# Performance work log

Hardware: AMD Instinct MI355X
Metric: run time of the kernel (lower is better)

Reference implementation:

```python
import jax, jax.numpy as jnp
import numpy as np

NUM_HEADS = 8
HEAD_DIM = 96
SCALE = HEAD_DIM ** -0.5
STRIDE_Q = (1, 2, 2)
STRIDE_KV = (1, 8, 8)
PAD = [(1, 1), (1, 1), (1, 1)]  # kernel 3 -> padding = 3//2 = 1


def _gelu_pool(t, w, stride, thw):
    """_pre_attention_pool -> GELU -> depthwise Conv3d -> _post_attention_pool.

    t: [B, H, L, hd] flattened tokens; thw = (T, Hs, Ws) with L = T*Hs*Ws.
    Returns pooled [B, H, L', hd] and new thw.
    """
    B, NH, L, C = t.shape
    T, Hs, Ws = thw
    x = t.reshape(B * NH, T, Hs, Ws, C).transpose(0, 4, 1, 2, 3)  # [B*NH, C, T, Hs, Ws]
    x = jax.nn.gelu(x, approximate=False)  # torch F.gelu default (erf)
    x = jax.lax.conv_general_dilated(
        x, w, window_strides=stride, padding=PAD,
        dimension_numbers=('NCDHW', 'OIDHW', 'NCDHW'),
        feature_group_count=C)  # depthwise: groups = head_dim
    new_thw = (x.shape[2], x.shape[3], x.shape[4])
    Lp = new_thw[0] * new_thw[1] * new_thw[2]
    x = x.reshape(B, NH, C, Lp).transpose(0, 1, 3, 2)  # [B, NH, L', C]
    return x, new_thw


def setup_inputs() -> dict:
    key = jax.random.key(0)
    ks = jax.random.split(key, 8)
    B, T, Hs, Ws, C = 2, 8, 56, 56, 768
    L = T * Hs * Ws
    s = 0.02
    return {
        'x': jax.random.normal(ks[0], (B, L, C), jnp.float32),
        'qkv_w': jax.random.normal(ks[1], (3 * C, C), jnp.float32) * s,
        'qkv_b': jnp.zeros((3 * C,), jnp.float32),
        'proj_w': jax.random.normal(ks[2], (C, C), jnp.float32) * s,
        'proj_b': jnp.zeros((C,), jnp.float32),
        'pool_q_w': jax.random.normal(ks[3], (HEAD_DIM, 1, 3, 3, 3), jnp.float32) * 0.1,
        'pool_k_w': jax.random.normal(ks[4], (HEAD_DIM, 1, 3, 3, 3), jnp.float32) * 0.1,
        'pool_v_w': jax.random.normal(ks[5], (HEAD_DIM, 1, 3, 3, 3), jnp.float32) * 0.1,
        't_size': T, 'h_size': Hs, 'w_size': Ws,
    }


def reference(x, qkv_w, qkv_b, proj_w, proj_b, pool_q_w, pool_k_w, pool_v_w,
              t_size, h_size, w_size):
    B, N, C = x.shape
    # fused qkv projection -> [3, B, heads, N, head_dim]
    qkv = (x @ qkv_w.T + qkv_b).reshape(B, N, 3, NUM_HEADS, C // NUM_HEADS)
    qkv = qkv.transpose(2, 0, 3, 1, 4)
    q, k, v = qkv[0], qkv[1], qkv[2]

    thw = (t_size, h_size, w_size)
    q, q_thw = _gelu_pool(q, pool_q_w, STRIDE_Q, thw)
    k, _ = _gelu_pool(k, pool_k_w, STRIDE_KV, thw)
    v, _ = _gelu_pool(v, pool_v_w, STRIDE_KV, thw)

    attn = jax.nn.softmax((q * SCALE) @ jnp.swapaxes(k, -2, -1), axis=-1)
    Nq = q.shape[2]
    out = (attn @ v + q)  # residual_pool=True (iMViT)
    out = out.transpose(0, 2, 1, 3).reshape(B, Nq, C)
    out = out @ proj_w.T + proj_b
    return out
```

## Files before the change

kernel.cpp:

```cpp
#include <hip/hip_runtime.h>
#include <cstdint>

#define NH 8
#define HD 96
#define CDIM 768
#define BQ 2
#define T0 8
#define H0 56
#define W0 56
#define L0 (T0*H0*W0)
#define HP_Q 28
#define WP_Q 28
#define LQ (T0*HP_Q*WP_Q)
#define HP_K 7
#define WP_K 7
#define LK (T0*HP_K*WP_K)
#define LKP 416
#define SCALE 0.10206207261596577f
#define NYC 20
#define MKV 6400

typedef __bf16 bf16;
typedef bf16 bf16x4 __attribute__((ext_vector_type(4)));
typedef bf16 bf16x8 __attribute__((ext_vector_type(8)));
typedef float f32x4 __attribute__((ext_vector_type(4)));
typedef float f4 __attribute__((ext_vector_type(4)));

#define GPTR(x) ((const __attribute__((address_space(1))) void*)(x))
#define LPTR(x) ((__attribute__((address_space(3))) void*)(x))

__device__ __forceinline__ float fast_gelu(float x) {
    float z = __builtin_fabsf(x) * 0.7071067811865476f;
    float p = 1.f + z*(0.278393f + z*(0.230389f + z*(0.000972f + z*0.078108f)));
    p = p * p;
    p = p * p;
    float e = 1.f - __builtin_amdgcn_rcpf(p);
    float erfv = (x < 0.f) ? -e : e;
    return 0.5f * x * (1.f + erfv);
}

#define NW4 442368
#define NP4 147456
__global__ void cvt_w(const f4* __restrict__ wq, const f4* __restrict__ wp,
                      bf16x4* __restrict__ wqo, bf16x4* __restrict__ wpo) {
    const long total = NW4 + NP4;
    long stride = (long)gridDim.x * blockDim.x;
    for (long i = (long)blockIdx.x * blockDim.x + threadIdx.x; i < total; i += stride) {
        f4 v; bf16x4* o;
        if (i < NW4) { v = wq[i]; o = wqo + i; }
        else         { v = wp[i - NW4]; o = wpo + (i - NW4); }
        bf16x4 t;
        t[0] = (bf16)v[0]; t[1] = (bf16)v[1]; t[2] = (bf16)v[2]; t[3] = (bf16)v[3];
        *o = t;
    }
}

__device__ __forceinline__ int cmap(int i) {
    return ((i + 1) / 3) * 8 + (i + 1) % 3 - 1;
}

template<int MODE>
__global__ __launch_bounds__(256) void gemm_f32a(
    const float* __restrict__ A, const bf16* __restrict__ B,
    const float* __restrict__ bias, bf16* __restrict__ Out,
    int M, int N, int K, int NBN)
{
    __shared__ uint8_t sh[2*24576];
    const int tid = threadIdx.x;
    const int lane = tid & 63;
    const int w = tid >> 6;
    const int wr = w >> 1, wc = w & 1;
    const int g = lane >> 4;
    const int ar = lane & 15;

    const int nwg = gridDim.x;
    const int q_ = nwg >> 3, r_ = nwg & 7;
    const int xcd = blockIdx.x & 7, off = blockIdx.x >> 3;
    const int swz = (xcd < r_ ? xcd*(q_+1) : r_*(q_+1) + (xcd - r_)*q_) + off;
    const long bn = swz % NBN, bm = swz / NBN;

    f32x4 acc[4][4];
#pragma unroll
    for (int i = 0; i < 4; ++i)
#pragma unroll
        for (int j = 0; j < 4; ++j) acc[i][j] = (f32x4){0.f,0.f,0.f,0.f};

    const int arow_s = tid >> 3;
    const int csa = (tid & 7) ^ (arow_s & 7);
    long aoff[4];
#pragma unroll
    for (int s = 0; s < 4; ++s) {
        int rA = (int)bm*128 + s*32 + arow_s;
        if (MODE == 2) {
            int b = rA / 3200; int r = rA - b*3200;
            int t = r / 400;  int rr = r - t*400;
            int yi = rr / NYC, xi = rr - yi*NYC;
            aoff[s] = ((long)b*L0 + (t*H0 + cmap(yi))*W0 + cmap(xi)) * (long)K;
        } else {
            aoff[s] = (long)rA * K;
        }
    }
    const int brow_s = tid >> 2;
    const int csb = (tid & 3) ^ ((tid >> 3) & 3);
    const bf16* Bg = B + (bn*128 + brow_s)*(long)K + csb*8;

    auto stage = [&](int buf, int kt) {
        uint8_t* base = sh + buf*24576;
#pragma unroll
        for (int s = 0; s < 4; ++s)
            __builtin_amdgcn_global_load_lds(GPTR(A + aoff[s] + kt*32 + csa*4),
                LPTR(base + s*4096 + tid*16), 16, 0, 0);
#pragma unroll
        for (int s = 0; s < 2; ++s)
            __builtin_amdgcn_global_load_lds(GPTR(Bg + (long)kt*32 + (long)s*64*K),
                LPTR(base + 16384 + s*4096 + tid*16), 16, 0, 0);
    };
    auto compute = [&](int buf) {
        const float* ldsA = (const float*)(sh + buf*24576);
        const bf16* ldsB = (const bf16*)(sh + buf*24576 + 16384);
        bf16x8 af[4], bfr[4];
#pragma unroll
        for (int i = 0; i < 4; ++i) {
            int R = wr*64 + i*16 + ar;
            f32x4 lo = *(const f32x4*)&ldsA[R*32 + (((2*g    ) ^ (R & 7))*4)];
            f32x4 hi = *(const f32x4*)&ldsA[R*32 + (((2*g + 1) ^ (R & 7))*4)];
            bf16x8 t;
            t[0] = (bf16)lo[0]; t[1] = (bf16)lo[1]; t[2] = (bf16)lo[2]; t[3] = (bf16)lo[3];
            t[4] = (bf16)hi[0]; t[5] = (bf16)hi[1]; t[6] = (bf16)hi[2]; t[7] = (bf16)hi[3];
            af[i] = t;
        }
#pragma unroll
        for (int j = 0; j < 4; ++j) {
            int R = wc*64 + j*16 + ar;
            bfr[j] = *(const bf16x8*)&ldsB[R*32 + ((g ^ ((R >> 1) & 3))*8)];
        }
        __builtin_amdgcn_s_setprio(1);
#pragma unroll
        for (int i = 0; i < 4; ++i)
#pragma unroll
            for (int j = 0; j < 4; ++j)
                acc[i][j] = __builtin_amdgcn_mfma_f32_16x16x32_bf16(af[i], bfr[j], acc[i][j], 0, 0, 0);
        __builtin_amdgcn_s_setprio(0);
    };

    const int nkt = K / 32;
    stage(0, 0);
    for (int kt = 0; kt < nkt; ++kt) {
        if (kt + 1 < nkt) {
            stage((kt + 1) & 1, kt + 1);
            asm volatile("s_waitcnt vmcnt(6)" ::: "memory");
        } else {
            asm volatile("s_waitcnt vmcnt(0)" ::: "memory");
        }
        __builtin_amdgcn_s_barrier();
        __builtin_amdgcn_sched_barrier(0);
        compute(kt & 1);
        __builtin_amdgcn_sched_barrier(0);
        __builtin_amdgcn_s_barrier();
    }

    bf16* tls = (bf16*)sh;
#pragma unroll
    for (int j = 0; j < 4; ++j) {
        const int colb = (int)bn*128 + wc*64 + j*16;
        const int lcol = wc*64 + j*16 + ar;
        const float bcol = bias[colb + ar];
#pragma unroll
        for (int i = 0; i < 4; ++i) {
            int lrow0 = wr*64 + i*16 + (g << 2);
#pragma unroll
            for (int r = 0; r < 4; ++r)
                tls[(lrow0 + r)*136 + lcol] = (bf16)fast_gelu(acc[i][j][r] + bcol);
        }
    }
    __syncthreads();
#pragma unroll
    for (int it = 0; it < 8; ++it) {
        int idx = it*256 + tid;
        int mloc = idx >> 4;
        int ck = idx & 15;
        bf16x8 v = *(const bf16x8*)&tls[mloc*136 + ck*8];
        int m = (int)bm*128 + mloc;
        int col = (int)bn*128 + ck*8;
        if (MODE == 0) {
            int nh = col / HD;
            int c = col - nh*HD;
            int bflag = m >= L0;
            int l = m - (bflag ? L0 : 0);
            size_t addr = ((size_t)(bflag*8 + nh)*L0 + l)*HD + c;
            *(bf16x8*)&Out[addr] = v;
        } else {
            int part = col / 768;
            int cb = col - part*768;
            int nh = cb / HD;
            int c = cb - nh*HD;
            int b = m / 3200; int r = m - b*3200;
            size_t addr = ((size_t)(part*16 + b*8 + nh)*3200 + r)*HD + c;
            *(bf16x8*)&Out[addr] = v;
        }
    }
}

__global__ __launch_bounds__(256) void gemm_proj(
    const bf16* __restrict__ A, const bf16* __restrict__ B,
    const float* __restrict__ bias, float* __restrict__ Out,
    int M, int N, int K, int NBN)
{
    __shared__ bf16 sh[2*16384];
    const int tid = threadIdx.x;
    const int lane = tid & 63;
    const int w = tid >> 6;
    const int wr = w >> 1, wc = w & 1;

    const int nwg = gridDim.x;
    const int q_ = nwg >> 3, r_ = nwg & 7;
    const int xcd = blockIdx.x & 7, off = blockIdx.x >> 3;
    const int swz = (xcd < r_ ? xcd*(q_+1) : r_*(q_+1) + (xcd - r_)*q_) + off;
    const long bn = swz % NBN, bm = swz / NBN;

    f32x4 acc[4][4];
#pragma unroll
    for (int i = 0; i < 4; ++i)
#pragma unroll
        for (int j = 0; j < 4; ++j) acc[i][j] = (f32x4){0.f,0.f,0.f,0.f};

    const int trow = tid >> 3;
    const int tchunk = (tid & 7) ^ (trow & 7);
    const bf16* Ag = A + (bm*128 + trow)*(long)K + tchunk*8;
    const bf16* Bg = B + (bn*128 + trow)*(long)K + tchunk*8;

    const int arow = lane & 15;
    const int g8 = (lane >> 4) * 8;
    const int aswz = (arow & 7) * 8;

    auto stage = [&](int buf, int kt) {
        bf16* ldsA = sh + buf*16384;
        bf16* ldsB = sh + buf*16384 + 8192;
#pragma unroll
        for (int s = 0; s < 4; ++s) {
            __builtin_amdgcn_global_load_lds(GPTR(Ag + (long)kt*64 + (long)s*32*K),
                                             LPTR(ldsA + s*2048 + tid*8), 16, 0, 0);
            __builtin_amdgcn_global_load_lds(GPTR(Bg + (long)kt*64 + (long)s*32*K),
                                             LPTR(ldsB + s*2048 + tid*8), 16, 0, 0);
        }
    };
    auto compute = [&](int buf) {
        const bf16* ldsA = sh + buf*16384;
        const bf16* ldsB = sh + buf*16384 + 8192;
#pragma unroll
        for (int kk = 0; kk < 2; ++kk) {
            bf16x8 af[4], bfr[4];
#pragma unroll
            for (int i = 0; i < 4; ++i)
                af[i] = *(const bf16x8*)&ldsA[(wr*64 + i*16 + arow)*64 + ((kk*32 + g8) ^ aswz)];
#pragma unroll
            for (int j = 0; j < 4; ++j)
                bfr[j] = *(const bf16x8*)&ldsB[(wc*64 + j*16 + arow)*64 + ((kk*32 + g8) ^ aswz)];
            __builtin_amdgcn_s_setprio(1);
#pragma unroll
            for (int i = 0; i < 4; ++i)
#pragma unroll
                for (int j = 0; j < 4; ++j)
                    acc[i][j] = __builtin_amdgcn_mfma_f32_16x16x32_bf16(af[i], bfr[j], acc[i][j], 0, 0, 0);
            __builtin_amdgcn_s_setprio(0);
        }
    };

    const int nkt = K / 64;
    stage(0, 0);
    for (int kt = 0; kt < nkt; ++kt) {
        if (kt + 1 < nkt) {
            stage((kt + 1) & 1, kt + 1);
            asm volatile("s_waitcnt vmcnt(8)" ::: "memory");
        } else {
            asm volatile("s_waitcnt vmcnt(0)" ::: "memory");
        }
        __builtin_amdgcn_s_barrier();
        __builtin_amdgcn_sched_barrier(0);
        compute(kt & 1);
        __builtin_amdgcn_sched_barrier(0);
        __builtin_amdgcn_s_barrier();
    }

#pragma unroll
    for (int j = 0; j < 4; ++j) {
        const int col = (int)bn*128 + wc*64 + j*16 + (lane & 15);
        const float bcol = bias[col];
#pragma unroll
        for (int i = 0; i < 4; ++i) {
            int row0 = (int)bm*128 + wr*64 + i*16 + ((lane>>4)<<2);
#pragma unroll
            for (int r = 0; r < 4; ++r)
                Out[(size_t)(row0 + r)*N + col] = acc[i][j][r] + bcol;
        }
    }
}

__global__ __launch_bounds__(256) void dwconv_q(
    const bf16* __restrict__ in, const float* __restrict__ w,
    bf16* __restrict__ out, int total)
{
    __shared__ float lw[27*HD];
    for (int i = threadIdx.x; i < 27*HD; i += 256) {
        int c = i / 27, tap = i % 27;
        lw[tap*HD + c] = w[i];
    }
    __syncthreads();
    int idx = blockIdx.x*256 + threadIdx.x;
    if (idx >= total) return;
    int c8 = idx % 12;
    int p = idx / 12;
    int xo = p % WP_Q;
    int yo = (p / WP_Q) % HP_Q;
    int bh = p / (WP_Q*HP_Q);
    const bf16* ip = in + (size_t)bh * L0 * HD + c8*8;

    float acc[T0][8];
#pragma unroll
    for (int t = 0; t < T0; ++t)
#pragma unroll
        for (int j = 0; j < 8; ++j) acc[t][j] = 0.f;

#pragma unroll
    for (int dy = 0; dy < 3; ++dy) {
        int y = yo*2 + dy - 1;
        if ((unsigned)y >= (unsigned)H0) continue;
#pragma unroll
        for (int dx = 0; dx < 3; ++dx) {
            int x = xo*2 + dx - 1;
            if ((unsigned)x >= (unsigned)W0) continue;
            float wreg[3][8];
#pragma unroll
            for (int dt = 0; dt < 3; ++dt)
#pragma unroll
                for (int j = 0; j < 8; ++j)
                    wreg[dt][j] = lw[(dt*9 + dy*3 + dx)*HD + c8*8 + j];
            const bf16* colp = ip + ((size_t)(y*W0 + x))*HD;
#pragma unroll
            for (int t = 0; t < T0; ++t) {
                bf16x8 v = *(const bf16x8*)(colp + (size_t)t*H0*W0*HD);
                float f[8];
#pragma unroll
                for (int j = 0; j < 8; ++j) f[j] = (float)v[j];
#pragma unroll
                for (int dt = 0; dt < 3; ++dt) {
                    int to = t - dt + 1;
                    if (to < 0 || to >= T0) continue;
#pragma unroll
                    for (int j = 0; j < 8; ++j)
                        acc[to][j] += wreg[dt][j] * f[j];
                }
            }
        }
    }

#pragma unroll
    for (int to = 0; to < T0; ++to) {
        int l = (to*HP_Q + yo)*WP_Q + xo;
        bf16x8 ov;
#pragma unroll
        for (int j = 0; j < 8; ++j) ov[j] = (bf16)acc[to][j];
        *(bf16x8*)&out[((size_t)bh*LQ + l)*HD + c8*8] = ov;
    }
}

__global__ __launch_bounds__(256) void dwconv_kv_all(
    const bf16* __restrict__ kv, const float* __restrict__ wk,
    const float* __restrict__ wv, bf16* __restrict__ kout, bf16* __restrict__ vtout)
{
    const int seg = blockIdx.x / 40;
    const int lb  = blockIdx.x % 40;
    const float* w = seg ? wv : wk;
    const bf16* in = kv + (size_t)seg * 16 * 3200 * HD;
    __shared__ float lw[27*HD];
    for (int i = threadIdx.x; i < 27*HD; i += 256) {
        int c = i / 27, tap = i % 27;
        lw[tap*HD + c] = w[i];
    }
    __syncthreads();

    if (lb >= 37) {
        int pid = (lb - 37)*256 + threadIdx.x;
        if (seg == 0) {
            for (int e = pid; e < 16*24*96; e += 768) {
                int bh = e / (24*96); int rem = e - bh*24*96;
                int l = LK + rem / 96; int c = rem % 96;
                kout[((size_t)bh*LKP + l)*HD + c] = (bf16)0.f;
            }
        } else {
            for (int e = pid; e < 16*96*24; e += 768) {
                int bh = e / (96*24); int rem = e - bh*96*24;
                int c = rem / 24; int l = LK + rem % 24;
                vtout[((size_t)bh*HD + c)*LKP + l] = (bf16)0.f;
            }
        }
        return;
    }

    int idx = lb*256 + threadIdx.x;
    if (idx >= 16*HP_K*WP_K*12) return;
    int c8 = idx % 12;
    int p = idx / 12;
    int xo = p % WP_K;
    int yo = (p / WP_K) % HP_K;
    int bh = p / (WP_K*HP_K);
    const bf16* ip = in + (size_t)bh * 3200 * HD + c8*8;

    float acc[T0][8];
#pragma unroll
    for (int t = 0; t < T0; ++t)
#pragma unroll
        for (int j = 0; j < 8; ++j) acc[t][j] = 0.f;

#pragma unroll
    for (int dy = 0; dy < 3; ++dy) {
        int yi = 3*yo + dy - 1;
        if ((unsigned)yi >= (unsigned)NYC) continue;
#pragma unroll
        for (int dx = 0; dx < 3; ++dx) {
            int xi = 3*xo + dx - 1;
            if ((unsigned)xi >= (unsigned)NYC) continue;
            float wreg[3][8];
#pragma unroll
            for (int dt = 0; dt < 3; ++dt)
#pragma unroll
                for (int j = 0; j < 8; ++j)
                    wreg[dt][j] = lw[(dt*9 + dy*3 + dx)*HD + c8*8 + j];
            const bf16* colp = ip + ((size_t)(yi*NYC + xi))*HD;
#pragma unroll
            for (int t = 0; t < T0; ++t) {
                bf16x8 v = *(const bf16x8*)(colp + (size_t)t*400*HD);
                float f[8];
#pragma unroll
                for (int j = 0; j < 8; ++j) f[j] = (float)v[j];
#pragma unroll
                for (int dt = 0; dt < 3; ++dt) {
                    int to = t - dt + 1;
                    if (to < 0 || to >= T0) continue;
#pragma unroll
                    for (int j = 0; j < 8; ++j)
                        acc[to][j] += wreg[dt][j] * f[j];
                }
            }
        }
    }

#pragma unroll
    for (int to = 0; to < T0; ++to) {
        int l = (to*HP_K + yo)*WP_K + xo;
        if (seg == 1) {
#pragma unroll
            for (int j = 0; j < 8; ++j)
                vtout[((size_t)bh*HD + c8*8 + j)*LKP + l] = (bf16)acc[to][j];
        } else {
            bf16x8 ov;
#pragma unroll
            for (int j = 0; j < 8; ++j) ov[j] = (bf16)acc[to][j];
            *(bf16x8*)&kout[((size_t)bh*LKP + l)*HD + c8*8] = ov;
        }
    }
}

__global__ __launch_bounds__(256) void attn_mfma(
    const bf16* __restrict__ q, const bf16* __restrict__ k,
    const bf16* __restrict__ vt, bf16* __restrict__ out)
{
    const int tid = threadIdx.x;
    const int lane = tid & 63;
    const int w = tid >> 6;
    const int col = lane & 15;
    const int g = lane >> 4;
    const int blk = blockIdx.x;
    const int qblk = blk % (LQ/64);
    const int bh = blk / (LQ/64);
    const int q0 = qblk*64 + w*16;

    const bf16* Qp  = q  + ((size_t)bh*LQ + q0)*HD;
    const bf16* Kp  = k  + (size_t)bh*LKP*HD;
    const bf16* VTp = vt + (size_t)bh*HD*LKP;

    bf16x8 qf[3];
#pragma unroll
    for (int c = 0; c < 3; ++c)
        qf[c] = *(const bf16x8*)&Qp[(size_t)col*HD + c*32 + g*8];

    f32x4 o[6];
#pragma unroll
    for (int t = 0; t < 6; ++t) o[t] = (f32x4){0.f,0.f,0.f,0.f};
    float lsum = 0.f;

    for (int kc = 0; kc < LKP/32; ++kc) {
        const int kvb = kc*32;
        uint32_t P[2][2];
#pragma unroll
        for (int s = 0; s < 2; ++s) {
            f32x4 acc = (f32x4){0.f,0.f,0.f,0.f};
#pragma unroll
            for (int c = 0; c < 3; ++c) {
                bf16x8 kf = *(const bf16x8*)&Kp[(size_t)(kvb + s*16 + col)*HD + c*32 + g*8];
                acc = __builtin_amdgcn_mfma_f32_16x16x32_bf16(kf, qf[c], acc, 0, 0, 0);
            }
            bf16x4 pb;
#pragma unroll
            for (int r = 0; r < 4; ++r) {
                int kv = kvb + s*16 + g*4 + r;
                float p = (kv < LK) ? __expf(acc[r]*SCALE) : 0.f;
                lsum += p;
                pb[r] = (bf16)p;
            }
            union { bf16x4 v; uint32_t u[2]; } pk; pk.v = pb;
            P[s][0] = pk.u[0]; P[s][1] = pk.u[1];
        }
        uint32_t sa0 = (g < 2) ? P[1][0] : P[0][0];
        uint32_t sa1 = (g < 2) ? P[1][1] : P[0][1];
        uint32_t tb0 = (g < 2) ? P[0][0] : P[1][0];
        uint32_t tb1 = (g < 2) ? P[0][1] : P[1][1];
        uint32_t R32_0 = (uint32_t)__shfl_xor((int)sa0, 32);
        uint32_t R32_1 = (uint32_t)__shfl_xor((int)sa1, 32);
        uint32_t R48_0 = (uint32_t)__shfl_xor((int)sa0, 48);
        uint32_t R48_1 = (uint32_t)__shfl_xor((int)sa1, 48);
        uint32_t R16_0 = (uint32_t)__shfl_xor((int)tb0, 16);
        uint32_t R16_1 = (uint32_t)__shfl_xor((int)tb1, 16);
        union { uint32_t u[4]; bf16x8 v; } pf;
        pf.u[0] = (g == 0) ? P[0][0] : (g == 1) ? R48_0 : (g == 2) ? R32_0 : R16_0;
        pf.u[1] = (g == 0) ? P[0][1] : (g == 1) ? R48_1 : (g == 2) ? R32_1 : R16_1;
        pf.u[2] = (g == 0) ? R16_0 : (g == 1) ? R32_0 : (g == 2) ? R48_0 : P[1][0];
        pf.u[3] = (g == 0) ? R16_1 : (g == 1) ? R32_1 : (g == 2) ? R48_1 : P[1][1];
#pragma unroll
        for (int t = 0; t < 6; ++t) {
            bf16x8 vf = *(const bf16x8*)&VTp[(size_t)(t*16 + col)*LKP + kvb + g*8];
            o[t] = __builtin_amdgcn_mfma_f32_16x16x32_bf16(vf, pf.v, o[t], 0, 0, 0);
        }
    }

    lsum += __shfl_xor(lsum, 16);
    lsum += __shfl_xor(lsum, 32);
    float inv = 1.f / lsum;

    const int b = bh >> 3, nh = bh & 7;
    size_t obase = ((size_t)b*LQ + q0 + col)*CDIM + (size_t)nh*HD;
#pragma unroll
    for (int t = 0; t < 6; ++t) {
        bf16x4 qres = *(const bf16x4*)&Qp[(size_t)col*HD + t*16 + g*4];
        bf16x4 ov;
#pragma unroll
        for (int r = 0; r < 4; ++r)
            ov[r] = (bf16)(o[t][r]*inv + (float)qres[r]);
        *(bf16x4*)&out[obase + t*16 + g*4] = ov;
    }
}

extern "C" void kernel_launch(void* const* d_in, const int* in_sizes, int n_in,
                              void* d_out, int out_size, void* d_ws, size_t ws_size,
                              hipStream_t stream) {
    const float* x      = (const float*)d_in[0];
    const float* qkv_w  = (const float*)d_in[1];
    const float* qkv_b  = (const float*)d_in[2];
    const float* proj_w = (const float*)d_in[3];
    const float* proj_b = (const float*)d_in[4];
    const float* pq_w   = (const float*)d_in[5];
    const float* pk_w   = (const float*)d_in[6];
    const float* pv_w   = (const float*)d_in[7];

    uint8_t* ws = (uint8_t*)d_ws;
    bf16* qg_out   = (bf16*)(ws);
    bf16* kv_c     = (bf16*)(ws +  77070336);
    bf16* wqkv_bf  = (bf16*)(ws +  96731136);
    bf16* wproj_bf = (bf16*)(ws + 100270080);
    bf16* q_bf     = (bf16*)(ws + 101449728);
    bf16* k_bf     = (bf16*)(ws + 120717312);
    bf16* vt_bf    = (bf16*)(ws + 121995264);
    bf16* attn_o   = (bf16*)(ws + 123273216);

    cvt_w<<<576, 256, 0, stream>>>((const f4*)qkv_w, (const f4*)proj_w,
                                   (bf16x4*)wqkv_bf, (bf16x4*)wproj_bf);

    gemm_f32a<0><<<392*6, 256, 0, stream>>>(
        x, wqkv_bf, qkv_b, qg_out, 50176, 768, 768, 6);

    gemm_f32a<2><<<50*12, 256, 0, stream>>>(
        x, wqkv_bf + (size_t)768*768, qkv_b + 768, kv_c, MKV, 1536, 768, 12);

    dwconv_q<<<588, 256, 0, stream>>>(qg_out, pq_w, q_bf, 16*HP_Q*WP_Q*12);
    dwconv_kv_all<<<80, 256, 0, stream>>>(kv_c, pk_w, pv_w, k_bf, vt_bf);

    attn_mfma<<<16*(LQ/64), 256, 0, stream>>>(q_bf, k_bf, vt_bf, attn_o);

    gemm_proj<<<6*98, 256, 0, stream>>>(
        attn_o, wproj_bf, proj_b, (float*)d_out, 12544, 768, 768, 6);
}
```

Baseline: 314.6 us.

## Merge Q and KV GEMMs and dwconv kernels into single launches; restructure pipelining

Combines the Q projection GEMM and the strided KV projection GEMM into one launch, with the block index choosing which problem each workgroup handles. The Q and KV depthwise-conv kernels are likewise merged into one launch. The double-buffered K loops in both GEMMs now wait for all loads, then issue the next stage after the barrier, which drops one barrier per iteration. The intent is fewer launches and less tail idle time, but waiting on vmcnt(0) before compute reduces the overlap between loads and math.

```diff
diff --git a/kernel.cpp b/kernel.cpp
--- a/kernel.cpp
+++ b/kernel.cpp
@@ -19,6 +19,8 @@
 #define SCALE 0.10206207261596577f
 #define NYC 20
 #define MKV 6400
+#define NBQ 2352
+#define NBKV 600
 
 typedef __bf16 bf16;
 typedef bf16 bf16x4 __attribute__((ext_vector_type(4)));
@@ -59,11 +61,10 @@
     return ((i + 1) / 3) * 8 + (i + 1) % 3 - 1;
 }
 
-template<int MODE>
-__global__ __launch_bounds__(256) void gemm_f32a(
-    const float* __restrict__ A, const bf16* __restrict__ B,
-    const float* __restrict__ bias, bf16* __restrict__ Out,
-    int M, int N, int K, int NBN)
+__global__ __launch_bounds__(256) void gemm_qkv(
+    const float* __restrict__ A, const bf16* __restrict__ Wq,
+    const float* __restrict__ bias_q, bf16* __restrict__ OutQ,
+    bf16* __restrict__ OutKV)
 {
     __shared__ uint8_t sh[2*24576];
     const int tid = threadIdx.x;
@@ -72,12 +73,19 @@
     const int wr = w >> 1, wc = w & 1;
     const int g = lane >> 4;
     const int ar = lane & 15;
+    const int K = 768;
 
     const int nwg = gridDim.x;
     const int q_ = nwg >> 3, r_ = nwg & 7;
     const int xcd = blockIdx.x & 7, off = blockIdx.x >> 3;
     const int swz = (xcd < r_ ? xcd*(q_+1) : r_*(q_+1) + (xcd - r_)*q_) + off;
-    const long bn = swz % NBN, bm = swz / NBN;
+
+    const bool isQ = swz < NBQ;
+    const int idx = isQ ? swz : swz - NBQ;
+    const int NBN = isQ ? 6 : 12;
+    const long bm = idx / NBN, bn = idx % NBN;
+    const bf16* B = isQ ? Wq : Wq + (size_t)768*768;
+    const float* bias = isQ ? bias_q : bias_q + 768;
 
     f32x4 acc[4][4];
 #pragma unroll
@@ -91,7 +99,7 @@
 #pragma unroll
     for (int s = 0; s < 4; ++s) {
         int rA = (int)bm*128 + s*32 + arow_s;
-        if (MODE == 2) {
+        if (!isQ) {
             int b = rA / 3200; int r = rA - b*3200;
             int t = r / 400;  int rr = r - t*400;
             int yi = rr / NYC, xi = rr - yi*NYC;
@@ -146,19 +154,16 @@
     const int nkt = K / 32;
     stage(0, 0);
     for (int kt = 0; kt < nkt; ++kt) {
-        if (kt + 1 < nkt) {
-            stage((kt + 1) & 1, kt + 1);
-            asm volatile("s_waitcnt vmcnt(6)" ::: "memory");
-        } else {
-            asm volatile("s_waitcnt vmcnt(0)" ::: "memory");
-        }
+        const int cur = kt & 1;
+        asm volatile("s_waitcnt vmcnt(0)" ::: "memory");
         __builtin_amdgcn_s_barrier();
         __builtin_amdgcn_sched_barrier(0);
-        compute(kt & 1);
+        if (kt + 1 < nkt) stage(cur ^ 1, kt + 1);
+        compute(cur);
         __builtin_amdgcn_sched_barrier(0);
-        __builtin_amdgcn_s_barrier();
-    }
-
+    }
+
+    __syncthreads();
     bf16* tls = (bf16*)sh;
 #pragma unroll
     for (int j = 0; j < 4; ++j) {
@@ -176,19 +181,19 @@
     __syncthreads();
 #pragma unroll
     for (int it = 0; it < 8; ++it) {
-        int idx = it*256 + tid;
-        int mloc = idx >> 4;
-        int ck = idx & 15;
+        int idx2 = it*256 + tid;
+        int mloc = idx2 >> 4;
+        int ck = idx2 & 15;
         bf16x8 v = *(const bf16x8*)&tls[mloc*136 + ck*8];
         int m = (int)bm*128 + mloc;
         int col = (int)bn*128 + ck*8;
-        if (MODE == 0) {
+        if (isQ) {
             int nh = col / HD;
             int c = col - nh*HD;
             int bflag = m >= L0;
             int l = m - (bflag ? L0 : 0);
             size_t addr = ((size_t)(bflag*8 + nh)*L0 + l)*HD + c;
-            *(bf16x8*)&Out[addr] = v;
+            *(bf16x8*)&OutQ[addr] = v;
         } else {
             int part = col / 768;
             int cb = col - part*768;
@@ -196,7 +201,7 @@
             int c = cb - nh*HD;
             int b = m / 3200; int r = m - b*3200;
             size_t addr = ((size_t)(part*16 + b*8 + nh)*3200 + r)*HD + c;
-            *(bf16x8*)&Out[addr] = v;
+            *(bf16x8*)&OutKV[addr] = v;
         }
     }
 }
@@ -269,17 +274,13 @@
     const int nkt = K / 64;
     stage(0, 0);
     for (int kt = 0; kt < nkt; ++kt) {
-        if (kt + 1 < nkt) {
-            stage((kt + 1) & 1, kt + 1);
-            asm volatile("s_waitcnt vmcnt(8)" ::: "memory");
-        } else {
-            asm volatile("s_waitcnt vmcnt(0)" ::: "memory");
-        }
+        const int cur = kt & 1;
+        asm volatile("s_waitcnt vmcnt(0)" ::: "memory");
         __builtin_amdgcn_s_barrier();
         __builtin_amdgcn_sched_barrier(0);
-        compute(kt & 1);
+        if (kt + 1 < nkt) stage(cur ^ 1, kt + 1);
+        compute(cur);
         __builtin_amdgcn_sched_barrier(0);
-        __builtin_amdgcn_s_barrier();
     }
 
 #pragma unroll
@@ -296,83 +297,84 @@
     }
 }
 
-__global__ __launch_bounds__(256) void dwconv_q(
-    const bf16* __restrict__ in, const float* __restrict__ w,
-    bf16* __restrict__ out, int total)
+__global__ __launch_bounds__(256) void dwconv_all(
+    const bf16* __restrict__ qin, const bf16* __restrict__ kv,
+    const float* __restrict__ wq, const float* __restrict__ wk,
+    const float* __restrict__ wv, bf16* __restrict__ qout,
+    bf16* __restrict__ kout, bf16* __restrict__ vtout)
 {
     __shared__ float lw[27*HD];
-    for (int i = threadIdx.x; i < 27*HD; i += 256) {
-        int c = i / 27, tap = i % 27;
-        lw[tap*HD + c] = w[i];
-    }
-    __syncthreads();
-    int idx = blockIdx.x*256 + threadIdx.x;
-    if (idx >= total) return;
-    int c8 = idx % 12;
-    int p = idx / 12;
-    int xo = p % WP_Q;
-    int yo = (p / WP_Q) % HP_Q;
-    int bh = p / (WP_Q*HP_Q);
-    const bf16* ip = in + (size_t)bh * L0 * HD + c8*8;
-
-    float acc[T0][8];
-#pragma unroll
-    for (int t = 0; t < T0; ++t)
-#pragma unroll
-        for (int j = 0; j < 8; ++j) acc[t][j] = 0.f;
-
-#pragma unroll
-    for (int dy = 0; dy < 3; ++dy) {
-        int y = yo*2 + dy - 1;
-        if ((unsigned)y >= (unsigned)H0) continue;
-#pragma unroll
-        for (int dx = 0; dx < 3; ++dx) {
-            int x = xo*2 + dx - 1;
-            if ((unsigned)x >= (unsigned)W0) continue;
-            float wreg[3][8];
-#pragma unroll
-            for (int dt = 0; dt < 3; ++dt)
-#pragma unroll
-                for (int j = 0; j < 8; ++j)
-                    wreg[dt][j] = lw[(dt*9 + dy*3 + dx)*HD + c8*8 + j];
-            const bf16* colp = ip + ((size_t)(y*W0 + x))*HD;
-#pragma unroll
-            for (int t = 0; t < T0; ++t) {
-                bf16x8 v = *(const bf16x8*)(colp + (size_t)t*H0*W0*HD);
-                float f[8];
-#pragma unroll
-                for (int j = 0; j < 8; ++j) f[j] = (float)v[j];
-#pragma unroll
-                for (int dt = 0; dt < 3; ++dt) {
-                    int to = t - dt + 1;
-                    if (to < 0 || to >= T0) continue;
+    const int blk = blockIdx.x;
+    if (blk < 588) {
+        for (int i = threadIdx.x; i < 27*HD; i += 256) {
+            int c = i / 27, tap = i % 27;
+            lw[tap*HD + c] = wq[i];
+        }
+        __syncthreads();
+        int idx = blk*256 + threadIdx.x;
+        if (idx >= 16*HP_Q*WP_Q*12) return;
+        int c8 = idx % 12;
+        int p = idx / 12;
+        int xo = p % WP_Q;
+        int yo = (p / WP_Q) % HP_Q;
+        int bh = p / (WP_Q*HP_Q);
+        const bf16* ip = qin + (size_t)bh * L0 * HD + c8*8;
+
+        float acc[T0][8];
+#pragma unroll
+        for (int t = 0; t < T0; ++t)
+#pragma unroll
+            for (int j = 0; j < 8; ++j) acc[t][j] = 0.f;
+
+#pragma unroll
+        for (int dy = 0; dy < 3; ++dy) {
+            int y = yo*2 + dy - 1;
+            if ((unsigned)y >= (unsigned)H0) continue;
+#pragma unroll
+            for (int dx = 0; dx < 3; ++dx) {
+                int x = xo*2 + dx - 1;
+                if ((unsigned)x >= (unsigned)W0) continue;
+                float wreg[3][8];
+#pragma unroll
+                for (int dt = 0; dt < 3; ++dt)
 #pragma unroll
                     for (int j = 0; j < 8; ++j)
-                        acc[to][j] += wreg[dt][j] * f[j];
+                        wreg[dt][j] = lw[(dt*9 + dy*3 + dx)*HD + c8*8 + j];
+                const bf16* colp = ip + ((size_t)(y*W0 + x))*HD;
+#pragma unroll
+                for (int t = 0; t < T0; ++t) {
+                    bf16x8 v = *(const bf16x8*)(colp + (size_t)t*H0*W0*HD);
+                    float f[8];
+#pragma unroll
+                    for (int j = 0; j < 8; ++j) f[j] = (float)v[j];
+#pragma unroll
+                    for (int dt = 0; dt < 3; ++dt) {
+                        int to = t - dt + 1;
+                        if (to < 0 || to >= T0) continue;
+#pragma unroll
+                        for (int j = 0; j < 8; ++j)
+                            acc[to][j] += wreg[dt][j] * f[j];
+                    }
                 }
             }
         }
-    }
-
-#pragma unroll
-    for (int to = 0; to < T0; ++to) {
-        int l = (to*HP_Q + yo)*WP_Q + xo;
-        bf16x8 ov;
-#pragma unroll
-        for (int j = 0; j < 8; ++j) ov[j] = (bf16)acc[to][j];
-        *(bf16x8*)&out[((size_t)bh*LQ + l)*HD + c8*8] = ov;
-    }
-}
-
-__global__ __launch_bounds__(256) void dwconv_kv_all(
-    const bf16* __restrict__ kv, const float* __restrict__ wk,
-    const float* __restrict__ wv, bf16* __restrict__ kout, bf16* __restrict__ vtout)
-{
-    const int seg = blockIdx.x / 40;
-    const int lb  = blockIdx.x % 40;
+
+#pragma unroll
+        for (int to = 0; to < T0; ++to) {
+            int l = (to*HP_Q + yo)*WP_Q + xo;
+            bf16x8 ov;
+#pragma unroll
+            for (int j = 0; j < 8; ++j) ov[j] = (bf16)acc[to][j];
+            *(bf16x8*)&qout[((size_t)bh*LQ + l)*HD + c8*8] = ov;
+        }
+        return;
+    }
+
+    const int kb = blk - 588;
+    const int seg = kb / 40;
+    const int lb  = kb % 40;
     const float* w = seg ? wv : wk;
     const bf16* in = kv + (size_t)seg * 16 * 3200 * HD;
-    __shared__ float lw[27*HD];
     for (int i = threadIdx.x; i < 27*HD; i += 256) {
         int c = i / 27, tap = i % 27;
         lw[tap*HD + c] = w[i];
@@ -575,14 +577,10 @@
     cvt_w<<<576, 256, 0, stream>>>((const f4*)qkv_w, (const f4*)proj_w,
                                    (bf16x4*)wqkv_bf, (bf16x4*)wproj_bf);
 
-    gemm_f32a<0><<<392*6, 256, 0, stream>>>(
-        x, wqkv_bf, qkv_b, qg_out, 50176, 768, 768, 6);
-
-    gemm_f32a<2><<<50*12, 256, 0, stream>>>(
-        x, wqkv_bf + (size_t)768*768, qkv_b + 768, kv_c, MKV, 1536, 768, 12);
-
-    dwconv_q<<<588, 256, 0, stream>>>(qg_out, pq_w, q_bf, 16*HP_Q*WP_Q*12);
-    dwconv_kv_all<<<80, 256, 0, stream>>>(kv_c, pk_w, pv_w, k_bf, vt_bf);
+    gemm_qkv<<<NBQ + NBKV, 256, 0, stream>>>(x, wqkv_bf, qkv_b, qg_out, kv_c);
+
+    dwconv_all<<<668, 256, 0, stream>>>(qg_out, kv_c, pq_w, pk_w, pv_w,
+                                        q_bf, k_bf, vt_bf);
 
     attn_mfma<<<16*(LQ/64), 256, 0, stream>>>(q_bf, k_bf, vt_bf, attn_o);
 
```

After: 301.2 us. 4.3% less time.
